# Kernel optimization log

Hardware: AMD Instinct MI355X
Metric: run time of the kernel (lower is better)

## Reference

```python
import jax, jax.numpy as jnp
import numpy as np

B, C, H, W = 16, 256, 32, 32
DIM = H * W  # LayerNorm/Linear dim == h*w per the rearrange in forward


def _conv1x1(x, w, b):
    # x: [b,c,h,w], w: [out,in] (1x1 kernel squeezed), b: [out]
    return jnp.einsum('bchw,oc->bohw', x, w) + b[None, :, None, None]


def _layernorm(x, g, b, eps=1e-5):
    mu = jnp.mean(x, axis=-1, keepdims=True)
    var = jnp.var(x, axis=-1, keepdims=True)
    return (x - mu) / jnp.sqrt(var + eps) * g + b


def setup_inputs() -> dict:
    key = jax.random.key(0)
    ks = jax.random.split(key, 12)
    n = jax.random.normal
    k_cdc = (2.0 / (2 * C)) ** 0.5   # kaiming_normal fan_in = 2C
    k_v = (2.0 / C) ** 0.5           # fan_in = C
    k_lin = (2.0 / DIM) ** 0.5       # fan_in = DIM
    return {
        'x_spa': n(ks[0], (B, C, H, W), jnp.float32),
        'x_freq': n(ks[1], (B, C, H, W), jnp.float32),
        'w_cdc': n(ks[2], (C, 2 * C), jnp.float32) * k_cdc,
        'b_cdc': jnp.zeros((C,), jnp.float32),
        'w_sv': n(ks[3], (C, C), jnp.float32) * k_v,
        'b_sv': jnp.zeros((C,), jnp.float32),
        'w_fv': n(ks[4], (C, C), jnp.float32) * k_v,
        'b_fv': jnp.zeros((C,), jnp.float32),
        'ln_w': jnp.ones((DIM,), jnp.float32),
        'ln_b': jnp.zeros((DIM,), jnp.float32),
        'w_qk': n(ks[5], (2 * DIM, DIM), jnp.float32) * k_lin,  # Linear(dim, 2*dim), no bias
        'w_spa': n(ks[6], (DIM, DIM), jnp.float32) * k_lin,
        'b_spa': jnp.zeros((DIM,), jnp.float32),
        'w_frq': n(ks[7], (DIM, DIM), jnp.float32) * k_lin,
        'b_frq': jnp.zeros((DIM,), jnp.float32),
    }


def reference(x_spa, x_freq, w_cdc, b_cdc, w_sv, b_sv, w_fv, b_fv,
              ln_w, ln_b, w_qk, w_spa, b_spa, w_frq, b_frq):
    b, c, h, w = x_spa.shape
    hw = h * w
    scale = hw ** (-0.5)
    v_spa = _conv1x1(x_spa, w_sv, b_sv).reshape(b, c, hw)
    v_freq = _conv1x1(x_freq, w_fv, b_fv).reshape(b, c, hw)
    x = _conv1x1(jnp.concatenate([x_spa, x_freq], axis=1), w_cdc, b_cdc).reshape(b, c, hw)
    x = _layernorm(x, ln_w, ln_b)
    qk = x @ w_qk.T                       # [b, c, 2*hw]
    q, k = jnp.split(qk, 2, axis=-1)      # each [b, c, hw]
    att = jnp.einsum('bcn,bcm->bnm', q, k) * scale   # q^T k over channels: [b, hw, hw]
    att_spa = jax.nn.softmax(att @ w_spa.T + b_spa, axis=-1)
    att_frq = jax.nn.softmax(att @ w_frq.T + b_frq, axis=-1)
    out_spa = x_spa + jnp.einsum('bcn,bnm->bcm', v_spa, att_spa).reshape(b, c, h, w)
    out_freq = x_freq + jnp.einsum('bcn,bnm->bcm', v_freq, att_frq).reshape(b, c, h, w)
    return out_spa, out_freq
```

## Files before the change

kernel.cpp:

```cpp
#include <hip/hip_runtime.h>
#include <hip/hip_bf16.h>

typedef __hip_bfloat16 bf16;
typedef __attribute__((ext_vector_type(8))) short bf16x8v;
typedef __attribute__((ext_vector_type(4))) float f32x4v;

__device__ __forceinline__ float bfbits2f(unsigned short h) {
    union { unsigned int u; float f; } v; v.u = ((unsigned int)h) << 16; return v.f;
}
__device__ __forceinline__ unsigned short f2bfbits(float f) {
    bf16 h = __float2bfloat16(f);
    unsigned short s;
    __builtin_memcpy(&s, &h, 2);
    return s;
}
__device__ __forceinline__ float load1_any(const void* p, long idx, bool f32) {
    if (f32) return ((const float*)p)[idx];
    return bfbits2f(((const unsigned short*)p)[idx]);
}
__device__ __forceinline__ float4 loadbf4(const bf16* p) {
    ushort4 u = *reinterpret_cast<const ushort4*>(p);
    return make_float4(bfbits2f(u.x), bfbits2f(u.y), bfbits2f(u.z), bfbits2f(u.w));
}
__device__ __forceinline__ void store_bf4(bf16* p, float a, float b, float c, float d) {
    ushort4 o;
    o.x = f2bfbits(a); o.y = f2bfbits(b); o.z = f2bfbits(c); o.w = f2bfbits(d);
    *reinterpret_cast<ushort4*>(p) = o;
}
__device__ __forceinline__ void gl16(const void* g, void* l) {
    __builtin_amdgcn_global_load_lds(
        (const __attribute__((address_space(1))) unsigned int*)g,
        (__attribute__((address_space(3))) unsigned int*)l, 16, 0, 0);
}

__global__ __launch_bounds__(1024)
void detect_kernel(const unsigned short* __restrict__ x, int* __restrict__ flag) {
    const int tid = threadIdx.x;
    int zc = 0, hc = 0;
    const uint4* xv = (const uint4*)x;
#pragma unroll
    for (int p = 0; p < 16; ++p) {
        uint4 v = xv[p * 1024 + tid];
        unsigned s0 = v.x & 0xFFFFu, s1 = v.y & 0xFFFFu;
        unsigned s2 = v.z & 0xFFFFu, s3 = v.w & 0xFFFFu;
        zc += (int)(s0 == 0) + (int)(s1 == 0) + (int)(s2 == 0) + (int)(s3 == 0);
        hc += (int)(((s0 >> 7) & 0xFFu) >= 0x90u) + (int)(((s1 >> 7) & 0xFFu) >= 0x90u)
            + (int)(((s2 >> 7) & 0xFFu) >= 0x90u) + (int)(((s3 >> 7) & 0xFFu) >= 0x90u);
    }
#pragma unroll
    for (int off = 32; off > 0; off >>= 1) {
        zc += __shfl_down(zc, off);
        hc += __shfl_down(hc, off);
    }
    __shared__ int rz[16], rh[16];
    if ((tid & 63) == 0) { rz[tid >> 6] = zc; rh[tid >> 6] = hc; }
    __syncthreads();
    if (tid == 0) {
        int Z = 0, H = 0;
#pragma unroll
        for (int i = 0; i < 16; ++i) { Z += rz[i]; H += rh[i]; }
        *flag = (Z > 60000 || H > 256) ? 1 : 0;
    }
}

__global__ void diag_kernel(float* __restrict__ out, float val) {
    if (threadIdx.x == 0) out[0] = val;
}

__global__ __launch_bounds__(256)
void convert6_kernel(const void* __restrict__ s0, const void* __restrict__ s1,
                     const void* __restrict__ s2, const void* __restrict__ s3,
                     const void* __restrict__ s4, const void* __restrict__ s5,
                     bf16* __restrict__ dst, const int* __restrict__ dflag) {
    const bool f32 = (*dflag != 0);
    for (long i = (long)blockIdx.x * 256 + threadIdx.x; i < 4456448;
         i += (long)gridDim.x * 256) {
        const void* s; long o;
        if (i < 131072)       { s = s0; o = i; }
        else if (i < 196608)  { s = s1; o = i - 131072; }
        else if (i < 262144)  { s = s2; o = i - 196608; }
        else if (i < 2359296) { s = s3; o = i - 262144; }
        else if (i < 3407872) { s = s4; o = i - 2359296; }
        else                  { s = s5; o = i - 3407872; }
        dst[i] = __float2bfloat16(load1_any(s, o, f32));
    }
}

__global__ __launch_bounds__(256)
void xpose_conv_kernel(const void* __restrict__ x1, const void* __restrict__ x2,
                       bf16* __restrict__ dst, int bofs, int zsplit,
                       const int* __restrict__ dflag) {
    const bool f32 = (*dflag != 0);
    __shared__ float t[64][65];
    const int ch0 = blockIdx.y * 64, n0 = blockIdx.x * 64, z = blockIdx.z;
    const bool hiz = (z >= zsplit);
    const int zl = hiz ? z - zsplit : z;
    const void* x = hiz ? x2 : x1;
    const long sb = (long)(zl + bofs) * 262144, db = (long)z * 262144;
    const int tid = threadIdx.x;
#pragma unroll
    for (int p = 0; p < 16; ++p) {
        int e = tid + p * 256; int sch = e >> 6, sn = e & 63;
        t[sch][sn] = load1_any(x, sb + (long)(ch0 + sch) * 1024 + n0 + sn, f32);
    }
    __syncthreads();
#pragma unroll
    for (int p = 0; p < 16; ++p) {
        int e = tid + p * 256; int dn = e >> 6, dch = e & 63;
        dst[db + (long)(n0 + dn) * 256 + ch0 + dch] = __float2bfloat16(t[dch][dn]);
    }
}

__global__ __launch_bounds__(256)
void smnorm_kernel(bf16* __restrict__ X, float* __restrict__ invS) {
    const int tid = threadIdx.x;
    const int cg = tid & 7;
    const int js = tid >> 3;
    const int n0 = blockIdx.x * 64;
    const long zb = (long)blockIdx.y * 1048576;
    unsigned short* Xp = (unsigned short*)X + zb + n0 + cg * 8;

    float m[8];
#pragma unroll
    for (int q = 0; q < 8; ++q) m[q] = -3.4e38f;
#pragma unroll 4
    for (int r = 0; r < 32; ++r) {
        bf16x8v u = *(const bf16x8v*)(Xp + (long)(js * 32 + r) * 1024);
#pragma unroll
        for (int q = 0; q < 8; ++q)
            m[q] = fmaxf(m[q], bfbits2f((unsigned short)u[q]));
    }
    __shared__ float sh[32][8][8];
    __shared__ float Mc[64];
#pragma unroll
    for (int q = 0; q < 8; ++q) sh[js][cg][q] = m[q];
    __syncthreads();
    if (tid < 64) {
        float mm = -3.4e38f;
#pragma unroll 8
        for (int s = 0; s < 32; ++s) mm = fmaxf(mm, sh[s][tid >> 3][tid & 7]);
        Mc[tid] = mm;
    }
    __syncthreads();
    float M8[8], s8[8];
#pragma unroll
    for (int q = 0; q < 8; ++q) { M8[q] = Mc[cg * 8 + q]; s8[q] = 0.f; }
#pragma unroll 4
    for (int r = 0; r < 32; ++r) {
        long off = (long)(js * 32 + r) * 1024;
        bf16x8v u = *(const bf16x8v*)(Xp + off);
        bf16x8v o;
#pragma unroll
        for (int q = 0; q < 8; ++q) {
            float e = __expf(bfbits2f((unsigned short)u[q]) - M8[q]);
            s8[q] += e;
            o[q] = (short)f2bfbits(e);
        }
        *(bf16x8v*)(Xp + off) = o;
    }
    __syncthreads();
#pragma unroll
    for (int q = 0; q < 8; ++q) sh[js][cg][q] = s8[q];
    __syncthreads();
    if (tid < 64) {
        float ss = 0.f;
#pragma unroll 8
        for (int s = 0; s < 32; ++s) ss += sh[s][tid >> 3][tid & 7];
        invS[(long)blockIdx.y * 1024 + n0 + tid] = 1.0f / ss;
    }
}

template <int EPI>
__global__ __launch_bounds__(256)
void mfma_nt(const bf16* __restrict__ A1, const bf16* __restrict__ A2,
             long aB1, long aB2, int ldA1, int ldA2,
             const bf16* __restrict__ B1, const bf16* __restrict__ B2,
             long bB1, long bB2, int ldB1, int ldB2,
             int ksplit, long kOff2,
             void* __restrict__ out1, void* __restrict__ out2,
             long oB1, long oB2, int ldO1, int ldO2,
             int K, float scale,
             const void* __restrict__ bias1, const void* __restrict__ bias2,
             const void* __restrict__ res1, const void* __restrict__ res2,
             long rBatch, int bofs, int zsplit, int swapXY,
             const int* __restrict__ dflag) {
    __shared__ short As[5][4096];
    __shared__ short Bs[5][4096];
    const int tid  = threadIdx.x;
    const int lane = tid & 63, wave = tid >> 6;
    const int quad = lane >> 4, lrow = lane & 15;
    const int wm = (wave >> 1) * 64, wn = (wave & 1) * 64;
    const int z  = blockIdx.z;
    const bool hiz = (z >= zsplit);
    const int zl = hiz ? z - zsplit : z;
    const bool sw = hiz && swapXY;
    const int n0 = (sw ? blockIdx.y : blockIdx.x) * 128;
    const int m0 = (sw ? blockIdx.x : blockIdx.y) * 128;
    const int ldA = hiz ? ldA2 : ldA1, ldB = hiz ? ldB2 : ldB1;
    const int ldO = hiz ? ldO2 : ldO1;
    const int srow = tid >> 2, sseg = tid & 3;
    const int sl = sseg ^ ((srow >> 1) & 3);
    const int xq = quad ^ ((lrow >> 1) & 3);

    const bf16* Ab = (hiz ? A2 : A1) + (long)zl * (hiz ? aB2 : aB1);
    const bf16* Bb = (hiz ? B2 : B1) + (long)zl * (hiz ? bB2 : bB1);

    auto stage = [&](int buf, int k0) {
        const bf16* asrc = Ab + (long)k0;
        const bf16* bsrc = Bb + ((k0 < ksplit) ? (long)k0 : (long)(k0 - ksplit) + kOff2);
        const bf16* ga0 = asrc + (long)(m0 + srow) * ldA + sl * 8;
        const bf16* ga1 = asrc + (long)(m0 + 64 + srow) * ldA + sl * 8;
        const bf16* gb0 = bsrc + (long)(n0 + srow) * ldB + sl * 8;
        const bf16* gb1 = bsrc + (long)(n0 + 64 + srow) * ldB + sl * 8;
        short* la = &As[buf][wave * 512];
        short* lb = &Bs[buf][wave * 512];
        gl16(ga0, la);
        gl16(ga1, la + 2048);
        gl16(gb0, lb);
        gl16(gb1, lb + 2048);
    };

    f32x4v acc[4][4] = {};
    const int nt = K >> 5;
    stage(0, 0);
    if (nt > 1) stage(1, 32);
    if (nt > 2) stage(2, 64);
    if (nt > 3) stage(3, 96);

    int cur = 0;
    for (int t = 0; t < nt; ++t) {
        const int rem = nt - 1 - t;
        if (rem >= 3)      asm volatile("s_waitcnt vmcnt(12)" ::: "memory");
        else if (rem == 2) asm volatile("s_waitcnt vmcnt(8)" ::: "memory");
        else if (rem == 1) asm volatile("s_waitcnt vmcnt(4)" ::: "memory");
        else               asm volatile("s_waitcnt vmcnt(0)" ::: "memory");
        __builtin_amdgcn_s_barrier();
        __builtin_amdgcn_sched_barrier(0);
        bf16x8v bfr[4], afr[4];
#pragma unroll
        for (int j = 0; j < 4; ++j)
            bfr[j] = *(const bf16x8v*)&Bs[cur][(wn + j * 16 + lrow) * 32 + xq * 8];
#pragma unroll
        for (int i = 0; i < 4; ++i)
            afr[i] = *(const bf16x8v*)&As[cur][(wm + i * 16 + lrow) * 32 + xq * 8];
        asm volatile("s_waitcnt lgkmcnt(0)" ::: "memory");
        __builtin_amdgcn_sched_barrier(0);
        if (t + 4 < nt) {
            int nb = cur + 4; if (nb >= 5) nb -= 5;
            stage(nb, (t + 4) << 5);
        }
#pragma unroll
        for (int i = 0; i < 4; ++i)
#pragma unroll
            for (int j = 0; j < 4; ++j)
                acc[i][j] = __builtin_amdgcn_mfma_f32_16x16x32_bf16(afr[i], bfr[j], acc[i][j], 0, 0, 0);
        cur = (cur == 4) ? 0 : cur + 1;
    }

    const bool f32 = (*dflag != 0);
    const void* bias = hiz ? bias2 : bias1;
    if (EPI != 3) {
        bf16* O = (bf16*)(hiz ? out2 : out1) + (long)zl * (hiz ? oB2 : oB1);
        const float* csp = (EPI == 4)
            ? (const float*)(hiz ? res2 : res1) + (long)zl * rBatch : nullptr;
#pragma unroll
        for (int i = 0; i < 4; ++i) {
            int row0 = m0 + wm + i * 16 + quad * 4;
            float rb[4] = {0.f, 0.f, 0.f, 0.f};
            if (EPI == 1 || EPI == 2 || EPI == 4) {
#pragma unroll
                for (int r = 0; r < 4; ++r) rb[r] = load1_any(bias, row0 + r, f32);
            }
#pragma unroll
            for (int j = 0; j < 4; ++j) {
                int col = n0 + wn + j * 16 + lrow;
                float cs = (EPI == 4) ? csp[col] : 1.0f;
#pragma unroll
                for (int r = 0; r < 4; ++r) {
                    float vv = acc[i][j][r];
                    if (EPI == 1) vv += rb[r];
                    if (EPI == 2) vv = vv * scale + rb[r];
                    if (EPI == 4) vv = (vv + rb[r]) * cs;
                    O[(long)(row0 + r) * ldO + col] = __float2bfloat16(vv);
                }
            }
        }
    } else {
        float* O = (float*)(hiz ? out2 : out1);
        const void* res = hiz ? res2 : res1;
        const long ob  = (long)(zl + bofs) * (hiz ? oB2 : oB1);
        const long rbb = (long)(zl + bofs) * rBatch;
#pragma unroll
        for (int i = 0; i < 4; ++i) {
            int row0 = m0 + wm + i * 16 + quad * 4;
#pragma unroll
            for (int j = 0; j < 4; ++j) {
                int col = n0 + wn + j * 16 + lrow;
#pragma unroll
                for (int r = 0; r < 4; ++r) {
                    float rv = load1_any(res, rbb + (long)(row0 + r) * ldO + col, f32);
                    O[ob + (long)(row0 + r) * ldO + col] = acc[i][j][r] + rv;
                }
            }
        }
    }
}

__global__ __launch_bounds__(256)
void layernorm_kernel(bf16* __restrict__ x, const void* __restrict__ g,
                      const void* __restrict__ beta, const int* __restrict__ dflag) {
    const bool f32 = (*dflag != 0);
    bf16* p = x + (long)blockIdx.x * 1024;
    const int tid = threadIdx.x;
    float4 v = loadbf4(p + tid * 4);
    float s  = v.x + v.y + v.z + v.w;
    float ss = v.x * v.x + v.y * v.y + v.z * v.z + v.w * v.w;
#pragma unroll
    for (int off = 32; off > 0; off >>= 1) {
        s  += __shfl_down(s, off);
        ss += __shfl_down(ss, off);
    }
    __shared__ float sh[8];
    __shared__ float sh_mu, sh_rs;
    if ((tid & 63) == 0) { sh[tid >> 6] = s; sh[4 + (tid >> 6)] = ss; }
    __syncthreads();
    if (tid == 0) {
        float S  = sh[0] + sh[1] + sh[2] + sh[3];
        float SS = sh[4] + sh[5] + sh[6] + sh[7];
        float mu = S * (1.0f / 1024.0f);
        float var = SS * (1.0f / 1024.0f) - mu * mu;
        sh_mu = mu;
        sh_rs = rsqrtf(fmaxf(var, 0.0f) + 1e-5f);
    }
    __syncthreads();
    float mu = sh_mu, rs = sh_rs;
    float gx = load1_any(g, tid * 4 + 0, f32), gy = load1_any(g, tid * 4 + 1, f32);
    float gz = load1_any(g, tid * 4 + 2, f32), gw = load1_any(g, tid * 4 + 3, f32);
    float bx = load1_any(beta, tid * 4 + 0, f32), by = load1_any(beta, tid * 4 + 1, f32);
    float bz = load1_any(beta, tid * 4 + 2, f32), bw = load1_any(beta, tid * 4 + 3, f32);
    store_bf4(p + tid * 4,
              (v.x - mu) * rs * gx + bx, (v.y - mu) * rs * gy + by,
              (v.z - mu) * rs * gz + bz, (v.w - mu) * rs * gw + bw);
}

extern "C" void kernel_launch(void* const* d_in, const int* in_sizes, int n_in,
                              void* d_out, int out_size, void* d_ws, size_t ws_size,
                              hipStream_t stream) {
    const void* x_spa  = d_in[0];
    const void* x_freq = d_in[1];
    const void* w_cdc  = d_in[2];
    const void* b_cdc  = d_in[3];
    const void* w_sv   = d_in[4];
    const void* b_sv   = d_in[5];
    const void* w_fv   = d_in[6];
    const void* b_fv   = d_in[7];
    const void* ln_w   = d_in[8];
    const void* ln_b   = d_in[9];
    const void* w_qk   = d_in[10];
    const void* w_spa  = d_in[11];
    const void* b_spa  = d_in[12];
    const void* w_frq  = d_in[13];
    const void* b_frq  = d_in[14];
    float* out = (float*)d_out;

    const int B = 16, C = 256;
    const long XB = 262144;
    const long PB = 1048576;

    int*  dflag = (int*)d_ws;
    bf16* wb    = (bf16*)((char*)d_ws + 4096);
    bf16* w_cdc_b = wb;
    bf16* w_sv_b  = w_cdc_b + 131072;
    bf16* w_fv_b  = w_sv_b  + 65536;
    bf16* w_qk_b  = w_fv_b  + 65536;
    bf16* w_spa_b = w_qk_b  + 2097152;
    bf16* w_frq_b = w_spa_b + 1048576;
    bf16* pb      = w_frq_b + 1048576;

    const size_t fixedB = 4096 + 4456448ull * 2;
    const size_t perB   = 8921088ull;
    size_t avail = (ws_size > fixedB) ? (ws_size - fixedB) : 0;
    long gmax = (long)(avail / perB);
    const bool wsOK = (gmax >= 1);
    int G = wsOK ? (int)(gmax > 16 ? 16 : gmax) : 1;

    bf16* xT    = pb;
    bf16* xln   = xT   + 2L * G * XB;
    bf16* kb    = xln  + (long)G * XB;
    bf16* qT    = kb   + (long)G * XB;
    bf16* TT    = qT   + (long)G * XB;
    bf16* vb    = TT   + 2L * G * XB;
    bf16* attpT = vb   + 2L * G * XB;
    float* invS = (float*)(attpT + 2L * G * PB);

    dim3 blk(256);
    detect_kernel<<<dim3(1), dim3(1024), 0, stream>>>((const unsigned short*)x_spa, dflag);

    if (!wsOK) {
        float mb = (float)(ws_size >> 20);
        diag_kernel<<<dim3(1), dim3(64), 0, stream>>>(out, 1000.0f * (mb + 1.0f));
        return;
    }

    convert6_kernel<<<dim3(4352), blk, 0, stream>>>(w_cdc, w_sv, w_fv, w_qk, w_spa, w_frq,
                                                    wb, dflag);

    for (int b0 = 0; b0 < B; b0 += G) {
        int g = (B - b0 < G) ? (B - b0) : G;

        xpose_conv_kernel<<<dim3(16, 4, 2 * g), blk, 0, stream>>>(
            x_spa, x_freq, xT, b0, g, dflag);

        mfma_nt<1><<<dim3(8, 2, g), blk, 0, stream>>>(
            w_cdc_b, w_cdc_b, 0, 0, 512, 512,
            xT, xT, XB, XB, 256, 256, 256, (long)g * XB,
            xln, xln, XB, XB, 1024, 1024,
            512, 1.0f, b_cdc, b_cdc, nullptr, nullptr, 0, 0, g, 0, dflag);
        layernorm_kernel<<<dim3(g * C), blk, 0, stream>>>(xln, ln_w, ln_b, dflag);

        mfma_nt<0><<<dim3(8, 2, 2 * g), blk, 0, stream>>>(
            xln, w_qk_b, XB, 0, 1024, 1024,
            w_qk_b + 1048576, xln, 0, XB, 1024, 1024, 1024, 0,
            kb, qT, XB, XB, 1024, 256,
            1024, 1.0f, nullptr, nullptr, nullptr, nullptr, 0, 0, g, 1, dflag);

        mfma_nt<0><<<dim3(2, 8, 2 * g), blk, 0, stream>>>(
            w_spa_b, w_frq_b, 0, 0, 1024, 1024,
            kb, kb, XB, XB, 1024, 1024, 1024, 0,
            TT, TT + (long)g * XB, XB, XB, 256, 256,
            1024, 1.0f, nullptr, nullptr, nullptr, nullptr, 0, 0, g, 0, dflag);

        mfma_nt<2><<<dim3(8, 8, 2 * g), blk, 0, stream>>>(
            TT, TT + (long)g * XB, XB, XB, 256, 256,
            qT, qT, XB, XB, 256, 256, 256, 0,
            attpT, attpT + (long)g * PB, PB, PB, 1024, 1024,
            256, 0.03125f, b_spa, b_frq, nullptr, nullptr, 0, 0, g, 0, dflag);

        smnorm_kernel<<<dim3(16, 2 * g), blk, 0, stream>>>(attpT, invS);

        mfma_nt<4><<<dim3(8, 2, 2 * g), blk, 0, stream>>>(
            w_sv_b, w_fv_b, 0, 0, 256, 256,
            xT, xT + (long)g * XB, XB, XB, 256, 256, 256, 0,
            vb, vb + (long)g * XB, XB, XB, 1024, 1024,
            256, 1.0f, b_sv, b_fv, invS, invS + (long)g * 1024, 1024, 0, g, 0, dflag);

        mfma_nt<3><<<dim3(8, 2, 2 * g), blk, 0, stream>>>(
            vb, vb + (long)g * XB, XB, XB, 1024, 1024,
            attpT, attpT + (long)g * PB, PB, PB, 1024, 1024, 1024, 0,
            out, out + 4194304, XB, XB, 1024, 1024,
            1024, 1.0f, nullptr, nullptr, x_spa, x_freq, XB, b0, g, 0, dflag);
    }
}
```

Before: 346.5 us.

## Precompose weights, fuse conv GEMMs, and shrink MFMA pipeline with variable tile height

Precomputes W_spa·W_qk_hi and W_frq·W_qk_hi once per call so that the k and T projections run as a single batched GEMM against the layernormed activations. The cdc, sv and fv 1x1 convolutions are merged into one GEMM with a block-structured concatenated weight, and the softmax column scaling moves into a separate vscale pass. The MFMA kernel becomes templated on tile height, drops from a 5-stage to a 3-stage LDS pipeline, and raises wave priority around the MFMA loop. In exchange the code adds setup kernels and a weight-product GEMM on every call, changes the rounding order of the bf16 products, and alters the buffer layouts.

```diff
diff --git a/kernel.cpp b/kernel.cpp
--- a/kernel.cpp
+++ b/kernel.cpp
@@ -59,7 +59,8 @@
         int Z = 0, H = 0;
 #pragma unroll
         for (int i = 0; i < 16; ++i) { Z += rz[i]; H += rh[i]; }
-        *flag = (Z > 60000 || H > 256) ? 1 : 0;
+        flag[0] = (Z > 60000 || H > 256) ? 1 : 0;
+        flag[1] = 1;
     }
 }
 
@@ -87,6 +88,48 @@
 }
 
 __global__ __launch_bounds__(256)
+void xpose_w_kernel(const bf16* __restrict__ src, bf16* __restrict__ dst) {
+    __shared__ float t[64][65];
+    const int c0 = blockIdx.x * 64, r0 = blockIdx.y * 64;
+    const int tid = threadIdx.x;
+#pragma unroll
+    for (int p = 0; p < 16; ++p) {
+        int e = tid + p * 256; int r = e >> 6, c = e & 63;
+        t[r][c] = __bfloat162float(src[(long)(r0 + r) * 1024 + c0 + c]);
+    }
+    __syncthreads();
+#pragma unroll
+    for (int p = 0; p < 16; ++p) {
+        int e = tid + p * 256; int r = e >> 6, c = e & 63;
+        dst[(long)(c0 + r) * 1024 + r0 + c] = __float2bfloat16(t[c][r]);
+    }
+}
+
+__global__ __launch_bounds__(256)
+void build_wleft_kernel(const bf16* __restrict__ w_cdc, const bf16* __restrict__ w_sv,
+                        const bf16* __restrict__ w_fv, bf16* __restrict__ W) {
+    int i = blockIdx.x * 256 + threadIdx.x;
+    if (i >= 393216) return;
+    int r = i >> 9, c = i & 511;
+    float v = 0.f;
+    if (r < 256) v = __bfloat162float(w_cdc[r * 512 + c]);
+    else if (r < 512) { if (c < 256) v = __bfloat162float(w_sv[(r - 256) * 256 + c]); }
+    else              { if (c >= 256) v = __bfloat162float(w_fv[(r - 512) * 256 + (c - 256)]); }
+    W[i] = __float2bfloat16(v);
+}
+
+__global__ __launch_bounds__(256)
+void build_bcat_kernel(const void* __restrict__ b0, const void* __restrict__ b1,
+                       const void* __restrict__ b2, float* __restrict__ bc,
+                       const int* __restrict__ dflag) {
+    const bool f32 = (*dflag != 0);
+    int i = blockIdx.x * 256 + threadIdx.x;
+    if (i < 256)      bc[i] = load1_any(b0, i, f32);
+    else if (i < 512) bc[i] = load1_any(b1, i - 256, f32);
+    else if (i < 768) bc[i] = load1_any(b2, i - 512, f32);
+}
+
+__global__ __launch_bounds__(256)
 void xpose_conv_kernel(const void* __restrict__ x1, const void* __restrict__ x2,
                        bf16* __restrict__ dst, int bofs, int zsplit,
                        const int* __restrict__ dflag) {
@@ -170,7 +213,22 @@
     }
 }
 
-template <int EPI>
+__global__ __launch_bounds__(256)
+void vscale_kernel(bf16* __restrict__ vb, const float* __restrict__ invS, int gN) {
+    long base = ((long)blockIdx.x * 256 + threadIdx.x) * 8;
+    if (base >= (long)512 * gN) return;
+    int r = (int)(base / gN);
+    long zn = base - (long)r * gN;
+    const float* is = invS + (long)(r >> 8) * gN + zn;
+    bf16x8v u = *(bf16x8v*)(vb + base);
+    bf16x8v o;
+#pragma unroll
+    for (int q = 0; q < 8; ++q)
+        o[q] = (short)f2bfbits(bfbits2f((unsigned short)u[q]) * is[q]);
+    *(bf16x8v*)(vb + base) = o;
+}
+
+template <int MI, int EPI>
 __global__ __launch_bounds__(256)
 void mfma_nt(const bf16* __restrict__ A1, const bf16* __restrict__ A2,
              long aB1, long aB2, int ldA1, int ldA2,
@@ -182,20 +240,19 @@
              int K, float scale,
              const void* __restrict__ bias1, const void* __restrict__ bias2,
              const void* __restrict__ res1, const void* __restrict__ res2,
-             long rBatch, int bofs, int zsplit, int swapXY,
+             long rBatch, int bofs, int zsplit,
              const int* __restrict__ dflag) {
-    __shared__ short As[5][4096];
-    __shared__ short Bs[5][4096];
+    constexpr int BM = MI * 32;
+    __shared__ short As[3][BM * 32];
+    __shared__ short Bs[3][4096];
     const int tid  = threadIdx.x;
     const int lane = tid & 63, wave = tid >> 6;
     const int quad = lane >> 4, lrow = lane & 15;
-    const int wm = (wave >> 1) * 64, wn = (wave & 1) * 64;
+    const int wm = (wave >> 1) * (MI * 16), wn = (wave & 1) * 64;
     const int z  = blockIdx.z;
     const bool hiz = (z >= zsplit);
     const int zl = hiz ? z - zsplit : z;
-    const bool sw = hiz && swapXY;
-    const int n0 = (sw ? blockIdx.y : blockIdx.x) * 128;
-    const int m0 = (sw ? blockIdx.x : blockIdx.y) * 128;
+    const int n0 = blockIdx.x * 128, m0 = blockIdx.y * BM;
     const int ldA = hiz ? ldA2 : ldA1, ldB = hiz ? ldB2 : ldB1;
     const int ldO = hiz ? ldO2 : ldO1;
     const int srow = tid >> 2, sseg = tid & 3;
@@ -208,79 +265,72 @@
     auto stage = [&](int buf, int k0) {
         const bf16* asrc = Ab + (long)k0;
         const bf16* bsrc = Bb + ((k0 < ksplit) ? (long)k0 : (long)(k0 - ksplit) + kOff2);
-        const bf16* ga0 = asrc + (long)(m0 + srow) * ldA + sl * 8;
-        const bf16* ga1 = asrc + (long)(m0 + 64 + srow) * ldA + sl * 8;
-        const bf16* gb0 = bsrc + (long)(n0 + srow) * ldB + sl * 8;
-        const bf16* gb1 = bsrc + (long)(n0 + 64 + srow) * ldB + sl * 8;
-        short* la = &As[buf][wave * 512];
-        short* lb = &Bs[buf][wave * 512];
-        gl16(ga0, la);
-        gl16(ga1, la + 2048);
-        gl16(gb0, lb);
-        gl16(gb1, lb + 2048);
+#pragma unroll
+        for (int p = 0; p < MI / 2; ++p)
+            gl16(asrc + (long)(m0 + p * 64 + srow) * ldA + sl * 8,
+                 &As[buf][p * 2048 + wave * 512]);
+        gl16(bsrc + (long)(n0 + srow) * ldB + sl * 8, &Bs[buf][wave * 512]);
+        gl16(bsrc + (long)(n0 + 64 + srow) * ldB + sl * 8, &Bs[buf][2048 + wave * 512]);
     };
 
-    f32x4v acc[4][4] = {};
+    f32x4v acc[MI][4] = {};
     const int nt = K >> 5;
     stage(0, 0);
     if (nt > 1) stage(1, 32);
-    if (nt > 2) stage(2, 64);
-    if (nt > 3) stage(3, 96);
 
     int cur = 0;
     for (int t = 0; t < nt; ++t) {
-        const int rem = nt - 1 - t;
-        if (rem >= 3)      asm volatile("s_waitcnt vmcnt(12)" ::: "memory");
-        else if (rem == 2) asm volatile("s_waitcnt vmcnt(8)" ::: "memory");
-        else if (rem == 1) asm volatile("s_waitcnt vmcnt(4)" ::: "memory");
-        else               asm volatile("s_waitcnt vmcnt(0)" ::: "memory");
+        if (t + 1 < nt) {
+            if constexpr (MI == 4) asm volatile("s_waitcnt vmcnt(4)" ::: "memory");
+            else                   asm volatile("s_waitcnt vmcnt(3)" ::: "memory");
+        } else {
+            asm volatile("s_waitcnt vmcnt(0)" ::: "memory");
+        }
         __builtin_amdgcn_s_barrier();
         __builtin_amdgcn_sched_barrier(0);
-        bf16x8v bfr[4], afr[4];
+        bf16x8v bfr[4], afr[MI];
 #pragma unroll
         for (int j = 0; j < 4; ++j)
             bfr[j] = *(const bf16x8v*)&Bs[cur][(wn + j * 16 + lrow) * 32 + xq * 8];
 #pragma unroll
-        for (int i = 0; i < 4; ++i)
+        for (int i = 0; i < MI; ++i)
             afr[i] = *(const bf16x8v*)&As[cur][(wm + i * 16 + lrow) * 32 + xq * 8];
         asm volatile("s_waitcnt lgkmcnt(0)" ::: "memory");
         __builtin_amdgcn_sched_barrier(0);
-        if (t + 4 < nt) {
-            int nb = cur + 4; if (nb >= 5) nb -= 5;
-            stage(nb, (t + 4) << 5);
+        if (t + 2 < nt) {
+            int nb = cur + 2; if (nb >= 3) nb -= 3;
+            stage(nb, (t + 2) << 5);
         }
-#pragma unroll
-        for (int i = 0; i < 4; ++i)
+        __builtin_amdgcn_s_setprio(1);
+#pragma unroll
+        for (int i = 0; i < MI; ++i)
 #pragma unroll
             for (int j = 0; j < 4; ++j)
                 acc[i][j] = __builtin_amdgcn_mfma_f32_16x16x32_bf16(afr[i], bfr[j], acc[i][j], 0, 0, 0);
-        cur = (cur == 4) ? 0 : cur + 1;
+        __builtin_amdgcn_s_setprio(0);
+        cur = (cur == 2) ? 0 : cur + 1;
     }
 
     const bool f32 = (*dflag != 0);
     const void* bias = hiz ? bias2 : bias1;
     if (EPI != 3) {
         bf16* O = (bf16*)(hiz ? out2 : out1) + (long)zl * (hiz ? oB2 : oB1);
-        const float* csp = (EPI == 4)
-            ? (const float*)(hiz ? res2 : res1) + (long)zl * rBatch : nullptr;
-#pragma unroll
-        for (int i = 0; i < 4; ++i) {
+#pragma unroll
+        for (int i = 0; i < MI; ++i) {
             int row0 = m0 + wm + i * 16 + quad * 4;
             float rb[4] = {0.f, 0.f, 0.f, 0.f};
-            if (EPI == 1 || EPI == 2 || EPI == 4) {
+            if (EPI == 1 || EPI == 2) {
 #pragma unroll
                 for (int r = 0; r < 4; ++r) rb[r] = load1_any(bias, row0 + r, f32);
             }
 #pragma unroll
             for (int j = 0; j < 4; ++j) {
                 int col = n0 + wn + j * 16 + lrow;
-                float cs = (EPI == 4) ? csp[col] : 1.0f;
 #pragma unroll
                 for (int r = 0; r < 4; ++r) {
                     float vv = acc[i][j][r];
                     if (EPI == 1) vv += rb[r];
                     if (EPI == 2) vv = vv * scale + rb[r];
-                    if (EPI == 4) vv = (vv + rb[r]) * cs;
                     O[(long)(row0 + r) * ldO + col] = __float2bfloat16(vv);
                 }
             }
@@ -291,7 +341,7 @@
         const long ob  = (long)(zl + bofs) * (hiz ? oB2 : oB1);
         const long rbb = (long)(zl + bofs) * rBatch;
 #pragma unroll
-        for (int i = 0; i < 4; ++i) {
+        for (int i = 0; i < MI; ++i) {
             int row0 = m0 + wm + i * 16 + quad * 4;
 #pragma unroll
             for (int j = 0; j < 4; ++j) {
@@ -307,10 +357,14 @@
 }
 
 __global__ __launch_bounds__(256)
-void layernorm_kernel(bf16* __restrict__ x, const void* __restrict__ g,
-                      const void* __restrict__ beta, const int* __restrict__ dflag) {
+void layernorm_kernel(const bf16* __restrict__ src, bf16* __restrict__ dst,
+                      const void* __restrict__ g, const void* __restrict__ beta,
+                      int gN, const int* __restrict__ dflag) {
     const bool f32 = (*dflag != 0);
-    bf16* p = x + (long)blockIdx.x * 1024;
+    const int zc = blockIdx.x;
+    const int zz = zc >> 8, c = zc & 255;
+    const bf16* p = src + (long)c * gN + (long)zz * 1024;
+    bf16* q = dst + (long)zc * 1024;
     const int tid = threadIdx.x;
     float4 v = loadbf4(p + tid * 4);
     float s  = v.x + v.y + v.z + v.w;
@@ -338,7 +392,7 @@
     float gz = load1_any(g, tid * 4 + 2, f32), gw = load1_any(g, tid * 4 + 3, f32);
     float bx = load1_any(beta, tid * 4 + 0, f32), by = load1_any(beta, tid * 4 + 1, f32);
     float bz = load1_any(beta, tid * 4 + 2, f32), bw = load1_any(beta, tid * 4 + 3, f32);
-    store_bf4(p + tid * 4,
+    store_bf4(q + tid * 4,
               (v.x - mu) * rs * gx + bx, (v.y - mu) * rs * gy + by,
               (v.z - mu) * rs * gz + bz, (v.w - mu) * rs * gw + bw);
 }
@@ -367,17 +421,21 @@
     const long XB = 262144;
     const long PB = 1048576;
 
-    int*  dflag = (int*)d_ws;
-    bf16* wb    = (bf16*)((char*)d_ws + 4096);
+    int*   dflag = (int*)d_ws;
+    float* bcat  = (float*)((char*)d_ws + 1024);
+    bf16*  wb    = (bf16*)((char*)d_ws + 4096);
     bf16* w_cdc_b = wb;
     bf16* w_sv_b  = w_cdc_b + 131072;
     bf16* w_fv_b  = w_sv_b  + 65536;
     bf16* w_qk_b  = w_fv_b  + 65536;
     bf16* w_spa_b = w_qk_b  + 2097152;
     bf16* w_frq_b = w_spa_b + 1048576;
-    bf16* pb      = w_frq_b + 1048576;
-
-    const size_t fixedB = 4096 + 4456448ull * 2;
+    bf16* w_qk_hiT= w_frq_b + 1048576;
+    bf16* W1f     = w_qk_hiT + 1048576;
+    bf16* Wleft   = W1f + 1048576;
+    bf16* pb      = Wleft + 393216;
+
+    const size_t fixedB = 4096 + 6946816ull * 2;
     const size_t perB   = 8921088ull;
     size_t avail = (ws_size > fixedB) ? (ws_size - fixedB) : 0;
     long gmax = (long)(avail / perB);
@@ -385,12 +443,10 @@
     int G = wsOK ? (int)(gmax > 16 ? 16 : gmax) : 1;
 
     bf16* xT    = pb;
-    bf16* xln   = xT   + 2L * G * XB;
-    bf16* kb    = xln  + (long)G * XB;
-    bf16* qT    = kb   + (long)G * XB;
-    bf16* TT    = qT   + (long)G * XB;
-    bf16* vb    = TT   + 2L * G * XB;
-    bf16* attpT = vb   + 2L * G * XB;
+    bf16* XV    = xT  + 2L * G * XB;
+    bf16* xln2  = XV  + 3L * G * XB;
+    bf16* qTT   = xln2 + (long)G * XB;
+    bf16* attpT = qTT + 3L * G * XB;
     float* invS = (float*)(attpT + 2L * G * PB);
 
     dim3 blk(256);
@@ -404,50 +460,51 @@
 
     convert6_kernel<<<dim3(4352), blk, 0, stream>>>(w_cdc, w_sv, w_fv, w_qk, w_spa, w_frq,
                                                     wb, dflag);
+    xpose_w_kernel<<<dim3(16, 16), blk, 0, stream>>>(w_qk_b + 1048576, w_qk_hiT);
+    build_wleft_kernel<<<dim3(1536), blk, 0, stream>>>(w_cdc_b, w_sv_b, w_fv_b, Wleft);
+    build_bcat_kernel<<<dim3(3), blk, 0, stream>>>(b_cdc, b_sv, b_fv, bcat, dflag);
+    mfma_nt<4, 0><<<dim3(8, 8, 2), blk, 0, stream>>>(
+        w_spa_b, w_frq_b, 0, 0, 1024, 1024,
+        w_qk_hiT, w_qk_hiT, 0, 0, 1024, 1024, 1024, 0,
+        w_qk_b + 1048576, W1f, 0, 0, 1024, 1024,
+        1024, 1.0f, nullptr, nullptr, nullptr, nullptr, 0, 0, 1, dflag);
 
     for (int b0 = 0; b0 < B; b0 += G) {
         int g = (B - b0 < G) ? (B - b0) : G;
+        const int gN = g * 1024;
+        bf16* vb = XV + 256L * gN;
 
         xpose_conv_kernel<<<dim3(16, 4, 2 * g), blk, 0, stream>>>(
             x_spa, x_freq, xT, b0, g, dflag);
 
-        mfma_nt<1><<<dim3(8, 2, g), blk, 0, stream>>>(
-            w_cdc_b, w_cdc_b, 0, 0, 512, 512,
-            xT, xT, XB, XB, 256, 256, 256, (long)g * XB,
-            xln, xln, XB, XB, 1024, 1024,
-            512, 1.0f, b_cdc, b_cdc, nullptr, nullptr, 0, 0, g, 0, dflag);
-        layernorm_kernel<<<dim3(g * C), blk, 0, stream>>>(xln, ln_w, ln_b, dflag);
-
-        mfma_nt<0><<<dim3(8, 2, 2 * g), blk, 0, stream>>>(
-            xln, w_qk_b, XB, 0, 1024, 1024,
-            w_qk_b + 1048576, xln, 0, XB, 1024, 1024, 1024, 0,
-            kb, qT, XB, XB, 1024, 256,
-            1024, 1.0f, nullptr, nullptr, nullptr, nullptr, 0, 0, g, 1, dflag);
-
-        mfma_nt<0><<<dim3(2, 8, 2 * g), blk, 0, stream>>>(
-            w_spa_b, w_frq_b, 0, 0, 1024, 1024,
-            kb, kb, XB, XB, 1024, 1024, 1024, 0,
-            TT, TT + (long)g * XB, XB, XB, 256, 256,
-            1024, 1.0f, nullptr, nullptr, nullptr, nullptr, 0, 0, g, 0, dflag);
-
-        mfma_nt<2><<<dim3(8, 8, 2 * g), blk, 0, stream>>>(
-            TT, TT + (long)g * XB, XB, XB, 256, 256,
-            qT, qT, XB, XB, 256, 256, 256, 0,
+        mfma_nt<4, 1><<<dim3(8 * g, 6, 1), blk, 0, stream>>>(
+            Wleft, Wleft, 0, 0, 512, 512,
+            xT, xT, 0, 0, 256, 256, 256, (long)g * XB,
+            XV, XV, 0, 0, gN, gN,
+            512, 1.0f, bcat, bcat, nullptr, nullptr, 0, 0, 1, dflag + 1);
+
+        layernorm_kernel<<<dim3(g * C), blk, 0, stream>>>(XV, xln2, ln_w, ln_b, gN, dflag);
+
+        mfma_nt<4, 0><<<dim3(2 * g, 8, 3), blk, 0, stream>>>(
+            w_qk_b, W1f, 1048576, 0, 1024, 1024,
+            xln2, xln2, 0, 0, 1024, 1024, 1024, 0,
+            qTT, qTT + 2L * g * XB, (long)g * XB, 0, g * 256, g * 256,
+            1024, 1.0f, nullptr, nullptr, nullptr, nullptr, 0, 0, 2, dflag);
+
+        mfma_nt<4, 2><<<dim3(8, 8, 2 * g), blk, 0, stream>>>(
+            qTT + (long)g * XB, qTT + 2L * g * XB, 256, 256, g * 256, g * 256,
+            qTT, qTT, 256, 256, g * 256, g * 256, 256, 0,
             attpT, attpT + (long)g * PB, PB, PB, 1024, 1024,
-            256, 0.03125f, b_spa, b_frq, nullptr, nullptr, 0, 0, g, 0, dflag);
+            256, 0.03125f, b_spa, b_frq, nullptr, nullptr, 0, 0, g, dflag);
 
         smnorm_kernel<<<dim3(16, 2 * g), blk, 0, stream>>>(attpT, invS);
 
-        mfma_nt<4><<<dim3(8, 2, 2 * g), blk, 0, stream>>>(
-            w_sv_b, w_fv_b, 0, 0, 256, 256,
-            xT, xT + (long)g * XB, XB, XB, 256, 256, 256, 0,
-            vb, vb + (long)g * XB, XB, XB, 1024, 1024,
-            256, 1.0f, b_sv, b_fv, invS, invS + (long)g * 1024, 1024, 0, g, 0, dflag);
-
-        mfma_nt<3><<<dim3(8, 2, 2 * g), blk, 0, stream>>>(
-            vb, vb + (long)g * XB, XB, XB, 1024, 1024,
+        vscale_kernel<<<dim3(gN / 4), blk, 0, stream>>>(vb, invS, gN);
+
+        mfma_nt<2, 3><<<dim3(8, 4, 2 * g), blk, 0, stream>>>(
+            vb, vb + 256L * gN, 1024, 1024, gN, gN,
             attpT, attpT + (long)g * PB, PB, PB, 1024, 1024, 1024, 0,
             out, out + 4194304, XB, XB, 1024, 1024,
-            1024, 1.0f, nullptr, nullptr, x_spa, x_freq, XB, b0, g, 0, dflag);
-    }
-}
+            1024, 1.0f, nullptr, nullptr, x_spa, x_freq, XB, b0, g, dflag);
+    }
+}
```

Result: no change. 349.8 us (+0.9%).
